# Optimization experiments

Hardware: AMD Instinct MI355X
Metric: run time of the kernel (lower is better)

## Reference

```python
import jax, jax.numpy as jnp
import numpy as np

N_HEAD = 16
N_KV_HEAD = 4
HD = 128
ROPE_THETA = 10000.0


def _rope_cos_sin(T, hd, dtype):
    inv_freq = 1.0 / (ROPE_THETA ** (jnp.arange(0, hd, 2, dtype=jnp.float32) / hd))  # [hd/2]
    ang = jnp.arange(T, dtype=jnp.float32)[:, None] * inv_freq[None, :]  # [T, hd/2]
    return jnp.cos(ang).astype(dtype), jnp.sin(ang).astype(dtype)


def _apply_rope(x, cos, sin):
    # x: [B, T, H, hd]; rotate interleaved (even, odd) pairs Llama-style
    x1 = x[..., 0::2]
    x2 = x[..., 1::2]
    c = cos[None, :, None, :]
    s = sin[None, :, None, :]
    o1 = x1 * c - x2 * s
    o2 = x1 * s + x2 * c
    return jnp.stack([o1, o2], axis=-1).reshape(x.shape)


def setup_inputs() -> dict:
    key = jax.random.key(0)
    k1, k2, k3 = jax.random.split(key, 3)
    B, T, C = 4, 2048, 2048
    x = jax.random.normal(k1, (B, T, C), dtype=jnp.float32)
    w_attn = jax.random.normal(k2, ((N_HEAD + 2 * N_KV_HEAD) * HD, C), dtype=jnp.float32) * (C ** -0.5)
    w_proj = jax.random.normal(k3, (C, C), dtype=jnp.float32) * (C ** -0.5)
    return {"x": x, "w_attn": w_attn, "w_proj": w_proj}


def reference(x, w_attn, w_proj):
    B, T, C = x.shape
    n_rep = N_HEAD // N_KV_HEAD
    qkv = x @ w_attn.T  # [B, T, (H + 2*Hkv)*hd]
    q, k, v = jnp.split(qkv, [N_HEAD * HD, (N_HEAD + N_KV_HEAD) * HD], axis=-1)
    q = q.reshape(B, T, N_HEAD, HD)
    k = k.reshape(B, T, N_KV_HEAD, HD)
    v = v.reshape(B, T, N_KV_HEAD, HD)
    cos, sin = _rope_cos_sin(T, HD, x.dtype)
    q = _apply_rope(q, cos, sin)
    k = _apply_rope(k, cos, sin)
    # GQA: repeat kv heads (repeat_interleave on head dim)
    k = jnp.repeat(k, n_rep, axis=2)
    v = jnp.repeat(v, n_rep, axis=2)
    # [B, H, T, hd]
    q = q.transpose(0, 2, 1, 3)
    k = k.transpose(0, 2, 1, 3)
    v = v.transpose(0, 2, 1, 3)
    att = jnp.einsum("bhqd,bhkd->bhqk", q, k) * (1.0 / jnp.sqrt(jnp.asarray(HD, x.dtype)))
    causal = jnp.tril(jnp.ones((T, T), dtype=bool))
    att = jnp.where(causal[None, None, :, :], att, jnp.asarray(-jnp.inf, att.dtype))
    att = jax.nn.softmax(att, axis=-1)
    y = jnp.einsum("bhqk,bhkd->bhqd", att, v)
    y = y.transpose(0, 2, 1, 3).reshape(B, T, C)
    return y @ w_proj.T
```

## Files before the change

kernel.cpp:

```cpp
#include <hip/hip_runtime.h>
#include <math.h>

#define NH   16
#define NKV  4
#define HD   128
#define BSZ  4
#define TLEN 2048
#define CDIM 2048
#define MROWS (BSZ*TLEN)

typedef short bf16x8 __attribute__((ext_vector_type(8)));
typedef float f32x4  __attribute__((ext_vector_type(4)));
typedef int   int4v  __attribute__((ext_vector_type(4)));

__device__ inline float bf2f(unsigned short h) {
  union { unsigned u; float f; } x; x.u = ((unsigned)h) << 16; return x.f;
}
__device__ inline unsigned short f2bf(float f) {
  union { float f; unsigned u; } x; x.f = f;
  unsigned u = x.u;
  return (unsigned short)((u + 0x7FFFu + ((u >> 16) & 1u)) >> 16);
}

__device__ inline void gload_lds16(const void* g, void* l) {
  __builtin_amdgcn_global_load_lds((const __attribute__((address_space(1))) void*)g,
                                   (__attribute__((address_space(3))) void*)l, 16, 0, 0);
}

__global__ void detect_kernel(const void* __restrict__ wproj, int* __restrict__ flag) {
  __shared__ int cnt;
  if (threadIdx.x == 0) cnt = 0;
  __syncthreads();
  const unsigned short* s = (const unsigned short*)wproj;
  unsigned short v = s[2 * threadIdx.x];
  int e = (v >> 7) & 0xFF;
  if (e >= 90 && e <= 141) atomicAdd(&cnt, 1);
  __syncthreads();
  if (threadIdx.x == 0) *flag = (cnt >= 192) ? 1 : 0;
}

__device__ inline void stage8(short* dst, const void* src, size_t eoff, int isbf) {
  if (isbf) {
    *(int4v*)dst = *(const int4v*)((const short*)src + eoff);
  } else {
    const f32x4* f = (const f32x4*)((const float*)src + eoff);
    f32x4 a = f[0], b = f[1];
    __align__(16) short t[8];
    t[0] = (short)f2bf(a[0]); t[1] = (short)f2bf(a[1]);
    t[2] = (short)f2bf(a[2]); t[3] = (short)f2bf(a[3]);
    t[4] = (short)f2bf(b[0]); t[5] = (short)f2bf(b[1]);
    t[6] = (short)f2bf(b[2]); t[7] = (short)f2bf(b[3]);
    *(int4v*)dst = *(int4v*)t;
  }
}

__global__ __launch_bounds__(256) void cvt_kernel(const void* __restrict__ src,
                                                  short* __restrict__ dst,
                                                  int n8, const int* __restrict__ flagp)
{
  const int fl = *flagp;
  const int i = blockIdx.x * 256 + threadIdx.x;
  if (i >= n8) return;
  __align__(16) short t[8];
  stage8(t, src, (size_t)i * 8, fl);
  *(int4v*)(dst + (size_t)i * 8) = *(int4v*)t;
}

template<int MODE>
__global__ __launch_bounds__(256) void gemm_bt(
    const short* __restrict__ A, const short* __restrict__ W,
    short* __restrict__ o0, short* __restrict__ o1, short* __restrict__ o2,
    float* __restrict__ o0f, const int* __restrict__ flagp)
{
  __shared__ __align__(16) short As[128*32];
  __shared__ __align__(16) short Bs[128*32];
  const int fl = *flagp;
  const int tid  = threadIdx.x;
  const int wave = tid >> 6;
  const int lane = tid & 63;
  const int cl   = lane & 15;
  const int quad = lane >> 4;
  const int m0 = blockIdx.y * 128;
  const int n0 = blockIdx.x * 128;
  const int wr = (wave >> 1) * 64;
  const int wc = (wave & 1) * 64;
  const int K = CDIM;
  const int rq = tid >> 2;
  const int cq = (tid & 3) << 3;
  const short* Ap = A + (size_t)(m0 + rq) * K + cq;
  const short* Wp = W + (size_t)(n0 + rq) * K + cq;
  short* AsW = As + wave * 512;
  short* BsW = Bs + wave * 512;
  const size_t rowskip = (size_t)64 * K;

  f32x4 acc[4][4];
#pragma unroll
  for (int i = 0; i < 4; i++)
#pragma unroll
    for (int j = 0; j < 4; j++) acc[i][j] = (f32x4){0.f, 0.f, 0.f, 0.f};

  for (int k0 = 0; k0 < K; k0 += 32) {
    gload_lds16(Ap + k0,           AsW);
    gload_lds16(Ap + k0 + rowskip, AsW + 2048);
    gload_lds16(Wp + k0,           BsW);
    gload_lds16(Wp + k0 + rowskip, BsW + 2048);
    __syncthreads();
    bf16x8 af[4], bfr[4];
#pragma unroll
    for (int i = 0; i < 4; i++) af[i]  = *(const bf16x8*)(&As[(wr + i*16 + cl)*32 + quad*8]);
#pragma unroll
    for (int j = 0; j < 4; j++) bfr[j] = *(const bf16x8*)(&Bs[(wc + j*16 + cl)*32 + quad*8]);
#pragma unroll
    for (int i = 0; i < 4; i++)
#pragma unroll
      for (int j = 0; j < 4; j++)
        acc[i][j] = __builtin_amdgcn_mfma_f32_16x16x32_bf16(af[i], bfr[j], acc[i][j], 0, 0, 0);
    __syncthreads();
  }

#pragma unroll
  for (int i = 0; i < 4; i++) {
#pragma unroll
    for (int j = 0; j < 4; j++) {
#pragma unroll
      for (int r = 0; r < 4; r++) {
        const int gm = m0 + wr + i*16 + quad*4 + r;
        const int gn = n0 + wc + j*16 + cl;
        const float fv = acc[i][j][r];
        if (MODE == 1) {
          if (fl) o0[(size_t)gm * CDIM + gn] = (short)f2bf(fv);
          else    o0f[(size_t)gm * CDIM + gn] = fv;
        } else {
          const int b = gm >> 11;
          const int t = gm & (TLEN - 1);
          const int head = gn >> 7;
          const int d = gn & (HD - 1);
          const unsigned short h = f2bf(fv);
          if (head < 16) {
            o0[(((size_t)(b*NH + head) * TLEN + t) << 7) + d] = (short)h;
          } else if (head < 20) {
            o1[(((size_t)(b*NKV + (head-16)) * TLEN + t) << 7) + d] = (short)h;
          } else {
            o2[(((size_t)(b*NKV + (head-20)) * HD + d) << 11) + t] = (short)h;
          }
        }
      }
    }
  }
}

__global__ __launch_bounds__(256) void rope_kernel(short* __restrict__ qb,
                                                   short* __restrict__ kb)
{
  const int idx = blockIdx.x * 256 + threadIdx.x;
  const int per_plane = TLEN * 64;
  const int plane = idx / per_plane;
  const int rem = idx - plane * per_plane;
  const int t = rem >> 6;
  const int i = rem & 63;
  short* base = (plane < 64) ? (qb + (size_t)plane * (TLEN*HD))
                             : (kb + (size_t)(plane - 64) * (TLEN*HD));
  const size_t off = (size_t)t * HD + 2*i;
  const float x1 = bf2f((unsigned short)base[off]);
  const float x2 = bf2f((unsigned short)base[off+1]);
  const float inv = __expf(-0.14391156847064198f * (float)i);
  const float ang = (float)t * inv;
  float s, c;
  sincosf(ang, &s, &c);
  base[off]   = (short)f2bf(x1*c - x2*s);
  base[off+1] = (short)f2bf(x1*s + x2*c);
}

__device__ inline void stage_tiles(short* Ks, short* Vs,
                                   const short* Kp, const short* Vp,
                                   int k0, int tid, int wave) {
#pragma unroll
  for (int i = 0; i < 4; i++) {
    const int chunk = i*256 + tid;
    const int row = chunk >> 4;
    const int cc  = (chunk & 15) ^ (row & 7);
    gload_lds16(Kp + (size_t)(k0 + row)*HD + cc*8,
                Ks + ((i*256 + wave*64) << 3));
  }
#pragma unroll
  for (int i = 0; i < 4; i++) {
    const int chunk = i*256 + tid;
    const int row = chunk >> 3;
    const int cc  = (chunk & 7) ^ (row & 7);
    gload_lds16(Vp + (size_t)row*TLEN + k0 + cc*8,
                Vs + ((i*256 + wave*64) << 3));
  }
}

__global__ __launch_bounds__(256) void attn_kernel(
    const short* __restrict__ qb, const short* __restrict__ kb,
    const short* __restrict__ vtb, short* __restrict__ yb)
{
  __shared__ __align__(16) short Ks[2][64*128];
  __shared__ __align__(16) short Vs[2][128*64];
  __shared__ short Plds[4][16][64];
  const int tid  = threadIdx.x;
  const int wave = tid >> 6;
  const int lane = tid & 63;
  const int cl   = lane & 15;
  const int quad = lane >> 4;
  const int bh = blockIdx.y;
  const int b = bh >> 4, h = bh & 15;
  const int kvh = h >> 2;

  const short* Qp = qb  + (size_t)(b*NH  + h)   * TLEN * HD;
  const short* Kp = kb  + (size_t)(b*NKV + kvh) * TLEN * HD;
  const short* Vp = vtb + (size_t)(b*NKV + kvh) * HD * TLEN;
  short* Pw = &Plds[wave][0][0];
  const int swz = (cl & 7) << 3;

  const float scale = 0.08838834764831845f;

#pragma unroll 1
  for (int pass = 0; pass < 2; ++pass) {
    const int qi = pass ? (TLEN/64 - 1 - (int)blockIdx.x) : (int)blockIdx.x;
    const int q0 = qi * 64;
    const int ntiles = qi + 1;

    bf16x8 qf[4];
    const int qrow = q0 + wave*16 + cl;
#pragma unroll
    for (int s = 0; s < 4; s++)
      qf[s] = *(const bf16x8*)(Qp + (size_t)qrow*HD + s*32 + quad*8);

    f32x4 O[8];
#pragma unroll
    for (int d = 0; d < 8; d++) O[d] = (f32x4){0.f, 0.f, 0.f, 0.f};
    float m_i[4], l_i[4];
#pragma unroll
    for (int r = 0; r < 4; r++) { m_i[r] = -1e9f; l_i[r] = 0.f; }

    stage_tiles(Ks[0], Vs[0], Kp, Vp, 0, tid, wave);
    __syncthreads();
    int cur = 0;

    for (int kt = 0; kt < ntiles; kt++) {
      const int k0 = kt * 64;

      if (kt + 1 < ntiles)
        stage_tiles(Ks[cur^1], Vs[cur^1], Kp, Vp, k0 + 64, tid, wave);

      const short* Kt = Ks[cur];
      const short* Vt = Vs[cur];

      f32x4 S[4];
#pragma unroll
      for (int j = 0; j < 4; j++) S[j] = (f32x4){0.f, 0.f, 0.f, 0.f};
#pragma unroll
      for (int s = 0; s < 4; s++) {
        bf16x8 kfj[4];
#pragma unroll
        for (int j = 0; j < 4; j++)
          kfj[j] = *(const bf16x8*)(&Kt[(size_t)(j*16 + cl)*128 + ((((s*4 + quad) << 3) ^ swz))]);
#pragma unroll
        for (int j = 0; j < 4; j++)
          S[j] = __builtin_amdgcn_mfma_f32_16x16x32_bf16(qf[s], kfj[j], S[j], 0, 0, 0);
      }

#pragma unroll
      for (int j = 0; j < 4; j++) {
        const int col = k0 + j*16 + cl;
#pragma unroll
        for (int r = 0; r < 4; r++) {
          const int row = q0 + wave*16 + quad*4 + r;
          const float sv = S[j][r] * scale;
          S[j][r] = (col <= row) ? sv : -1e9f;
        }
      }

      float alpha[4];
#pragma unroll
      for (int r = 0; r < 4; r++) {
        float mx = fmaxf(fmaxf(S[0][r], S[1][r]), fmaxf(S[2][r], S[3][r]));
#pragma unroll
        for (int off = 1; off < 16; off <<= 1) mx = fmaxf(mx, __shfl_xor(mx, off));
        const float mnew = fmaxf(m_i[r], mx);
        alpha[r] = __expf(m_i[r] - mnew);
        float rs = 0.f;
#pragma unroll
        for (int j = 0; j < 4; j++) {
          const float p = __expf(S[j][r] - mnew);
          S[j][r] = p;
          rs += p;
        }
#pragma unroll
        for (int off = 1; off < 16; off <<= 1) rs += __shfl_xor(rs, off);
        l_i[r] = l_i[r] * alpha[r] + rs;
        m_i[r] = mnew;
      }
#pragma unroll
      for (int d = 0; d < 8; d++)
#pragma unroll
        for (int r = 0; r < 4; r++) O[d][r] *= alpha[r];

#pragma unroll
      for (int j = 0; j < 4; j++)
#pragma unroll
        for (int r = 0; r < 4; r++) {
          const int row = quad*4 + r;
          int idx = row*64 + j*16 + cl;
          idx ^= (row & 7) << 3;
          Pw[idx] = (short)f2bf(S[j][r]);
        }

#pragma unroll
      for (int s2 = 0; s2 < 2; s2++) {
        int idx = cl*64 + s2*32 + quad*8;
        idx ^= (cl & 7) << 3;
        bf16x8 pf = *(const bf16x8*)(&Pw[idx]);
#pragma unroll
        for (int d = 0; d < 8; d++) {
          bf16x8 vfd = *(const bf16x8*)(&Vt[(size_t)(d*16 + cl)*64 + ((((s2*4 + quad) << 3) ^ swz))]);
          O[d] = __builtin_amdgcn_mfma_f32_16x16x32_bf16(pf, vfd, O[d], 0, 0, 0);
        }
      }

      __syncthreads();
      cur ^= 1;
    }

#pragma unroll
    for (int d = 0; d < 8; d++) {
#pragma unroll
      for (int r = 0; r < 4; r++) {
        const int t = q0 + wave*16 + quad*4 + r;
        const float v = O[d][r] / l_i[r];
        yb[(size_t)(b*TLEN + t) * CDIM + h*HD + d*16 + cl] = (short)f2bf(v);
      }
    }
  }
}

extern "C" void kernel_launch(void* const* d_in, const int* in_sizes, int n_in,
                              void* d_out, int out_size, void* d_ws, size_t ws_size,
                              hipStream_t stream)
{
  const void* x      = d_in[0];
  const void* w_attn = d_in[1];
  const void* w_proj = d_in[2];

  char* ws = (char*)d_ws;
  int*   flag = (int*)ws;
  short* qb  = (short*)(ws + (size_t) 1*1024*1024);
  short* kb  = (short*)(ws + (size_t)33*1024*1024);
  short* vtb = (short*)(ws + (size_t)41*1024*1024);
  short* yb  = (short*)(ws + (size_t)49*1024*1024);
  short* xb  = (short*)d_out;
  short* wab = (short*)((char*)d_out + (size_t)32*1024*1024);
  short* wpb = kb;

  dim3 blk(256);
  detect_kernel<<<1, blk, 0, stream>>>(w_proj, flag);
  cvt_kernel<<<dim3((MROWS*CDIM/8)/256), blk, 0, stream>>>(x, xb, MROWS*CDIM/8, flag);
  cvt_kernel<<<dim3((3072*CDIM/8)/256), blk, 0, stream>>>(w_attn, wab, 3072*CDIM/8, flag);
  gemm_bt<0><<<dim3(3072/128, MROWS/128), blk, 0, stream>>>(xb, wab, qb, kb, vtb, nullptr, flag);
  rope_kernel<<<dim3((80*TLEN*64)/256), blk, 0, stream>>>(qb, kb);
  attn_kernel<<<dim3(TLEN/128, BSZ*NH), blk, 0, stream>>>(qb, kb, vtb, yb);
  cvt_kernel<<<dim3((CDIM*CDIM/8)/256), blk, 0, stream>>>(w_proj, wpb, CDIM*CDIM/8, flag);
  gemm_bt<1><<<dim3(CDIM/128, MROWS/128), blk, 0, stream>>>(yb, wpb, (short*)d_out,
                                                            nullptr, nullptr, (float*)d_out, flag);
}
```

Baseline: 617.0 us.

## Add lazy softmax rescaling, diagonal-only masking, folded q-scale and GEMM block swizzle

```diff
diff --git a/kernel.cpp b/kernel.cpp
--- a/kernel.cpp
+++ b/kernel.cpp
@@ -80,8 +80,12 @@
   const int lane = tid & 63;
   const int cl   = lane & 15;
   const int quad = lane >> 4;
-  const int m0 = blockIdx.y * 128;
-  const int n0 = blockIdx.x * 128;
+  const int nwgx = gridDim.x;
+  int wg = (int)blockIdx.y * nwgx + (int)blockIdx.x;
+  const int cpx = (nwgx * (int)gridDim.y) >> 3;
+  wg = (wg & 7) * cpx + (wg >> 3);
+  const int m0 = (wg / nwgx) * 128;
+  const int n0 = (wg % nwgx) * 128;
   const int wr = (wave >> 1) * 64;
   const int wc = (wave & 1) * 64;
   const int K = CDIM;
@@ -167,8 +171,9 @@
   const float ang = (float)t * inv;
   float s, c;
   sincosf(ang, &s, &c);
-  base[off]   = (short)f2bf(x1*c - x2*s);
-  base[off+1] = (short)f2bf(x1*s + x2*c);
+  const float qscale = (plane < 64) ? 0.08838834764831845f : 1.0f;
+  base[off]   = (short)f2bf((x1*c - x2*s) * qscale);
+  base[off+1] = (short)f2bf((x1*s + x2*c) * qscale);
 }
 
 __device__ inline void stage_tiles(short* Ks, short* Vs,
@@ -214,8 +219,6 @@
   short* Pw = &Plds[wave][0][0];
   const int swz = (cl & 7) << 3;
 
-  const float scale = 0.08838834764831845f;
-
 #pragma unroll 1
   for (int pass = 0; pass < 2; ++pass) {
     const int qi = pass ? (TLEN/64 - 1 - (int)blockIdx.x) : (int)blockIdx.x;
@@ -262,41 +265,52 @@
           S[j] = __builtin_amdgcn_mfma_f32_16x16x32_bf16(qf[s], kfj[j], S[j], 0, 0, 0);
       }
 
-#pragma unroll
-      for (int j = 0; j < 4; j++) {
-        const int col = k0 + j*16 + cl;
-#pragma unroll
-        for (int r = 0; r < 4; r++) {
-          const int row = q0 + wave*16 + quad*4 + r;
-          const float sv = S[j][r] * scale;
-          S[j][r] = (col <= row) ? sv : -1e9f;
-        }
-      }
-
-      float alpha[4];
+      if (kt == ntiles - 1) {
+#pragma unroll
+        for (int j = 0; j < 4; j++) {
+          const int col = k0 + j*16 + cl;
+#pragma unroll
+          for (int r = 0; r < 4; r++) {
+            const int row = q0 + wave*16 + quad*4 + r;
+            if (col > row) S[j][r] = -1e9f;
+          }
+        }
+      }
+
+      float pmax[4];
 #pragma unroll
       for (int r = 0; r < 4; r++) {
         float mx = fmaxf(fmaxf(S[0][r], S[1][r]), fmaxf(S[2][r], S[3][r]));
 #pragma unroll
         for (int off = 1; off < 16; off <<= 1) mx = fmaxf(mx, __shfl_xor(mx, off));
-        const float mnew = fmaxf(m_i[r], mx);
-        alpha[r] = __expf(m_i[r] - mnew);
+        pmax[r] = mx;
+      }
+      const int ok = (pmax[0] - m_i[0] <= 8.f) && (pmax[1] - m_i[1] <= 8.f) &&
+                     (pmax[2] - m_i[2] <= 8.f) && (pmax[3] - m_i[3] <= 8.f);
+      if (!__all(ok)) {
+#pragma unroll
+        for (int r = 0; r < 4; r++) {
+          const float mnew = fmaxf(m_i[r], pmax[r]);
+          const float alpha = __expf(m_i[r] - mnew);
+          l_i[r] *= alpha;
+          m_i[r] = mnew;
+#pragma unroll
+          for (int d = 0; d < 8; d++) O[d][r] *= alpha;
+        }
+      }
+#pragma unroll
+      for (int r = 0; r < 4; r++) {
         float rs = 0.f;
 #pragma unroll
         for (int j = 0; j < 4; j++) {
-          const float p = __expf(S[j][r] - mnew);
+          const float p = __expf(S[j][r] - m_i[r]);
           S[j][r] = p;
           rs += p;
         }
 #pragma unroll
         for (int off = 1; off < 16; off <<= 1) rs += __shfl_xor(rs, off);
-        l_i[r] = l_i[r] * alpha[r] + rs;
-        m_i[r] = mnew;
-      }
-#pragma unroll
-      for (int d = 0; d < 8; d++)
-#pragma unroll
-        for (int r = 0; r < 4; r++) O[d][r] *= alpha[r];
+        l_i[r] += rs;
+      }
 
 #pragma unroll
       for (int j = 0; j < 4; j++)
@@ -324,13 +338,15 @@
       cur ^= 1;
     }
 
+    float linv[4];
+#pragma unroll
+    for (int r = 0; r < 4; r++) linv[r] = 1.0f / l_i[r];
 #pragma unroll
     for (int d = 0; d < 8; d++) {
 #pragma unroll
       for (int r = 0; r < 4; r++) {
         const int t = q0 + wave*16 + quad*4 + r;
-        const float v = O[d][r] / l_i[r];
-        yb[(size_t)(b*TLEN + t) * CDIM + h*HD + d*16 + cl] = (short)f2bf(v);
+        yb[(size_t)(b*TLEN + t) * CDIM + h*HD + d*16 + cl] = (short)f2bf(O[d][r] * linv[r]);
       }
     }
   }
```

Result: faster. 592.4 us (-4.0%).
